# Kernel tuning notes

Hardware: AMD Instinct MI355X
Metric: run time of the kernel (lower is better)

Reference implementation:

```python
import jax, jax.numpy as jnp
import numpy as np

B, T = 64, 32768
N_PROT = 18          # protein channels (len(steady_state))
N_PROLIF = 12        # prolif-hill library terms
N_LIN = 18           # lin-hill library terms (== len(sigmoid_sign))
N_TERMS = 1 + N_PROLIF + N_LIN  # 31


def setup_inputs() -> dict:
    key = jax.random.key(0)
    ks = jax.random.split(key, 8)
    candidates = jax.random.uniform(ks[0], (B, T, 4 + N_PROT), dtype=jnp.float32)
    a = jax.random.normal(ks[1], (N_TERMS,), dtype=jnp.float32)
    steady_state = jax.random.uniform(ks[2], (N_PROT,), dtype=jnp.float32) * 0.5
    # +/-1 signs, mimicking the hard-coded sign vector in the original module
    sigmoid_sign = jnp.where(
        jax.random.bernoulli(ks[3], 0.5, (N_LIN,)), 1.0, -1.0
    ).astype(jnp.float32)
    K1 = jnp.array([0.5], dtype=jnp.float32)
    theta = jnp.array([2.0], dtype=jnp.float32)
    K2 = jnp.array([0.3], dtype=jnp.float32)
    # library indices: cols 0,1 of prolif and col 0 of lin index x (4 channels);
    # col 2 of prolif and col 1 of lin index proteins (18 channels)
    prolif_hill_idx = jnp.stack(
        [
            jax.random.randint(ks[4], (N_PROLIF,), 0, 4),
            jax.random.randint(jax.random.fold_in(ks[4], 1), (N_PROLIF,), 0, 4),
            jax.random.randint(jax.random.fold_in(ks[4], 2), (N_PROLIF,), 0, N_PROT),
        ],
        axis=1,
    ).astype(jnp.int32)
    lin_hill_idx = jnp.stack(
        [
            jax.random.randint(ks[5], (N_LIN,), 0, 4),
            jax.random.randint(jax.random.fold_in(ks[5], 1), (N_LIN,), 0, N_PROT),
        ],
        axis=1,
    ).astype(jnp.int32)
    self_propagate = jax.random.bernoulli(ks[6], 0.5, (N_TERMS,))
    return {
        "candidates": candidates,
        "a": a,
        "steady_state": steady_state,
        "sigmoid_sign": sigmoid_sign,
        "K1": K1,
        "theta": theta,
        "K2": K2,
        "prolif_hill_idx": prolif_hill_idx,
        "lin_hill_idx": lin_hill_idx,
        "self_propagate": self_propagate,
    }


def reference(candidates, a, steady_state, sigmoid_sign, K1, theta, K2,
              prolif_hill_idx, lin_hill_idx, self_propagate):
    con = candidates[:, :, 0:1]                       # [B,T,1]
    x3 = candidates[:, :, 1:4]                        # [B,T,3]
    proteins = candidates[:, :, 4:]                   # [B,T,18]
    d_prot = proteins - steady_state                  # [B,T,18]
    # augment x with its sum -> 4 channels
    x = jnp.concatenate([x3, jnp.sum(x3, axis=2, keepdims=True)], axis=2)

    # prolif-hill terms: Log_term(x_i, x_j) * Hill(K1, protein_k)
    p0 = x[:, :, prolif_hill_idx[:, 0]]
    p1 = x[:, :, prolif_hill_idx[:, 1]]
    p2 = proteins[:, :, prolif_hill_idx[:, 2]]
    prolif_hill = p0 * (1.0 - p1 / theta) * (p2 / (K1 + p2))  # [B,T,12]

    # lin-hill terms: x_i * Hill(K2, |d_prot_j|) * sharp_sigmoid(sign * d_prot_j)
    l0 = x[:, :, lin_hill_idx[:, 0]]
    dp = d_prot[:, :, lin_hill_idx[:, 1]]
    adp = jnp.abs(dp)
    sig = jax.nn.sigmoid(500.0 * (sigmoid_sign * dp - 0.05))
    lin_hill = l0 * (adp / (K2 + adp)) * sig                  # [B,T,18]

    terms = jnp.concatenate([con, prolif_hill, lin_hill], axis=2)  # [B,T,31]

    # masked zero-out: keep term i iff (self_propagate[i] and a[i] >= 0)
    # or (not self_propagate[i] and a[i] <= 0)
    keep = jnp.where(self_propagate, a >= 0.0, a <= 0.0)
    terms = terms * keep.astype(terms.dtype)

    return terms @ a  # [B,T]
```

## Files before the change

### kernel.cpp

```cpp
#include <hip/hip_runtime.h>

#define NPROLIF 12
#define NLIN 18
#define ROW 22
#define BLK 256
#define F4_PER_BLK (BLK*ROW/4)
#define NSLAB 8192

#define AS1 __attribute__((address_space(1)))
#define AS3 __attribute__((address_space(3)))

__device__ __forceinline__ float sel4(unsigned i, float x0, float x1, float x2, float x3) {
    float lo = (i & 1u) ? x1 : x0;
    float hi = (i & 1u) ? x3 : x2;
    return (i & 2u) ? hi : lo;
}

__global__ __launch_bounds__(BLK) void sindy_kernel(
    const float* __restrict__ cand,
    const float* __restrict__ a,
    const float* __restrict__ ss,
    const float* __restrict__ sgn,
    const float* __restrict__ K1p,
    const float* __restrict__ thetap,
    const float* __restrict__ K2p,
    const int* __restrict__ pidx,
    const int* __restrict__ lidx,
    const int* __restrict__ sprop,
    float* __restrict__ out)
{
    __shared__ float sRow[BLK*ROW];
    __shared__ uint2 sPP[NPROLIF];
    __shared__ uint4 sLP[NLIN];
    __shared__ float sScal[4];

    const int tid = threadIdx.x;
    const int wbase = tid & ~63;

    const int slab = ((blockIdx.x & 7) << 10) | (blockIdx.x >> 3);

    const float4* g4 = reinterpret_cast<const float4*>(cand)
                       + (long long)slab * F4_PER_BLK;
    float4* s4 = reinterpret_cast<float4*>(sRow);
    #pragma unroll
    for (int k = 0; k < 5; ++k) {
        __builtin_amdgcn_global_load_lds(
            (const AS1 void*)(g4 + k*BLK + tid),
            (AS3 void*)(s4 + k*BLK + wbase), 16, 0, 0);
    }
    if (tid < F4_PER_BLK - 5*BLK) {
        __builtin_amdgcn_global_load_lds(
            (const AS1 void*)(g4 + 5*BLK + tid),
            (AS3 void*)(s4 + 5*BLK + wbase), 16, 0, 0);
    }

    if (tid < NPROLIF) {
        int i = tid;
        int ia = pidx[i*3+0], ib = pidx[i*3+1], ic = pidx[i*3+2];
        float av = a[1+i];
        bool keep = sprop[1+i] ? (av >= 0.f) : (av <= 0.f);
        unsigned offs = (unsigned)ia | ((unsigned)ib << 2) | ((unsigned)(16 + ic*4) << 8);
        sPP[i] = make_uint2(offs, __float_as_uint(keep ? av : 0.f));
    } else if (tid < NPROLIF + NLIN) {
        int j = tid - NPROLIF;
        int i0 = lidx[j*2+0], i1 = lidx[j*2+1];
        float av = a[1+NPROLIF+j];
        bool keep = sprop[1+NPROLIF+j] ? (av >= 0.f) : (av <= 0.f);
        unsigned offs = (unsigned)i0 | ((unsigned)(16 + i1*4) << 8);
        sLP[j] = make_uint4(offs,
                            __float_as_uint(keep ? av : 0.f),
                            __float_as_uint(500.f * sgn[j]),
                            __float_as_uint(ss[i1]));
    } else if (tid == NPROLIF + NLIN) {
        float av = a[0];
        bool keep = sprop[0] ? (av >= 0.f) : (av <= 0.f);
        sScal[0] = K1p[0];
        sScal[1] = 1.0f / thetap[0];
        sScal[2] = K2p[0];
        sScal[3] = keep ? av : 0.f;
    }

    __syncthreads();

    const char* row = (const char*)&sRow[tid*ROW];
    float con = sRow[tid*ROW+0];
    float x0  = sRow[tid*ROW+1];
    float x1  = sRow[tid*ROW+2];
    float x2  = sRow[tid*ROW+3];
    float xs  = x0 + x1 + x2;

    const float K1 = sScal[0], invTh = sScal[1], K2 = sScal[2];
    float acc = sScal[3] * con;

    #pragma unroll
    for (int i = 0; i < NPROLIF; ++i) {
        uint2 pp = sPP[i];
        float coef = __uint_as_float(pp.y);
        float pA = sel4(pp.x & 3u, x0, x1, x2, xs);
        float pB = sel4((pp.x >> 2) & 3u, x0, x1, x2, xs);
        float pC = *(const float*)(row + ((pp.x >> 8) & 0xffu));
        float h  = pC * __builtin_amdgcn_rcpf(K1 + pC);
        acc += coef * (pA * (1.0f - pB * invTh) * h);
    }

    #pragma unroll
    for (int j = 0; j < NLIN; ++j) {
        uint4 lp = sLP[j];
        float coef = __uint_as_float(lp.y);
        float A    = __uint_as_float(lp.z);
        float ssv  = __uint_as_float(lp.w);
        float l0 = sel4(lp.x & 3u, x0, x1, x2, xs);
        float pr = *(const float*)(row + ((lp.x >> 8) & 0xffu));
        float dp  = pr - ssv;
        float adp = fabsf(dp);
        float h   = adp * __builtin_amdgcn_rcpf(K2 + adp);
        float z   = A * dp - 25.0f;
        float e   = __expf(-z);
        float sig = __builtin_amdgcn_rcpf(1.0f + e);
        acc += coef * (l0 * h * sig);
    }

    out[(long long)slab * BLK + tid] = acc;
}

extern "C" void kernel_launch(void* const* d_in, const int* in_sizes, int n_in,
                              void* d_out, int out_size, void* d_ws, size_t ws_size,
                              hipStream_t stream) {
    const float* cand = (const float*)d_in[0];
    const float* a    = (const float*)d_in[1];
    const float* ss   = (const float*)d_in[2];
    const float* sgn  = (const float*)d_in[3];
    const float* K1   = (const float*)d_in[4];
    const float* th   = (const float*)d_in[5];
    const float* K2   = (const float*)d_in[6];
    const int*   pidx = (const int*)d_in[7];
    const int*   lidx = (const int*)d_in[8];
    const int*   sp   = (const int*)d_in[9];
    float* out = (float*)d_out;

    hipLaunchKernelGGL(sindy_kernel, dim3(NSLAB), dim3(BLK), 0, stream,
                       cand, a, ss, sgn, K1, th, K2, pidx, lidx, sp, out);
}
```

Baseline: 44.55 us.

## Use persistent blocks with register-prefetched next slab overlapping compute

Replaces the one-slab-per-block launch with a fixed grid of persistent blocks that loop over slabs. Each block prefetches the next slab into registers while computing the current one, then copies it to LDS between barriers. This replaces the direct global-to-LDS async loads and drops the blockIdx swizzle. It aims to hide load latency and amortise per-block setup, but adds register pressure and two barriers per iteration.

```diff
diff --git a/kernel.cpp b/kernel.cpp
--- a/kernel.cpp
+++ b/kernel.cpp
@@ -4,11 +4,9 @@
 #define NLIN 18
 #define ROW 22
 #define BLK 256
-#define F4_PER_BLK (BLK*ROW/4)
 #define NSLAB 8192
-
-#define AS1 __attribute__((address_space(1)))
-#define AS3 __attribute__((address_space(3)))
+#define GRID 1536
+#define F4_PER_SLAB (BLK*ROW/4)
 
 __device__ __forceinline__ float sel4(unsigned i, float x0, float x1, float x2, float x3) {
     float lo = (i & 1u) ? x1 : x0;
@@ -35,92 +33,107 @@
     __shared__ float sScal[4];
 
     const int tid = threadIdx.x;
-    const int wbase = tid & ~63;
+    const int bid = blockIdx.x;
 
-    const int slab = ((blockIdx.x & 7) << 10) | (blockIdx.x >> 3);
-
-    const float4* g4 = reinterpret_cast<const float4*>(cand)
-                       + (long long)slab * F4_PER_BLK;
-    float4* s4 = reinterpret_cast<float4*>(sRow);
-    #pragma unroll
-    for (int k = 0; k < 5; ++k) {
-        __builtin_amdgcn_global_load_lds(
-            (const AS1 void*)(g4 + k*BLK + tid),
-            (AS3 void*)(s4 + k*BLK + wbase), 16, 0, 0);
-    }
-    if (tid < F4_PER_BLK - 5*BLK) {
-        __builtin_amdgcn_global_load_lds(
-            (const AS1 void*)(g4 + 5*BLK + tid),
-            (AS3 void*)(s4 + 5*BLK + wbase), 16, 0, 0);
-    }
+    const int niter = (NSLAB - bid + GRID - 1) / GRID;
 
     if (tid < NPROLIF) {
-        int i = tid;
-        int ia = pidx[i*3+0], ib = pidx[i*3+1], ic = pidx[i*3+2];
-        float av = a[1+i];
-        bool keep = sprop[1+i] ? (av >= 0.f) : (av <= 0.f);
+        int t = tid;
+        int ia = pidx[t*3+0], ib = pidx[t*3+1], ic = pidx[t*3+2];
+        unsigned avb  = __float_as_uint(a[1+t]);
+        unsigned keep = ((sprop[1+t] != 0) ? 1u : 0u) ^ (avb >> 31);
         unsigned offs = (unsigned)ia | ((unsigned)ib << 2) | ((unsigned)(16 + ic*4) << 8);
-        sPP[i] = make_uint2(offs, __float_as_uint(keep ? av : 0.f));
+        sPP[t] = make_uint2(offs, keep ? avb : 0u);
     } else if (tid < NPROLIF + NLIN) {
         int j = tid - NPROLIF;
         int i0 = lidx[j*2+0], i1 = lidx[j*2+1];
-        float av = a[1+NPROLIF+j];
-        bool keep = sprop[1+NPROLIF+j] ? (av >= 0.f) : (av <= 0.f);
+        unsigned avb  = __float_as_uint(a[1+NPROLIF+j]);
+        unsigned keep = ((sprop[1+NPROLIF+j] != 0) ? 1u : 0u) ^ (avb >> 31);
         unsigned offs = (unsigned)i0 | ((unsigned)(16 + i1*4) << 8);
-        sLP[j] = make_uint4(offs,
-                            __float_as_uint(keep ? av : 0.f),
-                            __float_as_uint(500.f * sgn[j]),
-                            __float_as_uint(ss[i1]));
+        unsigned A = 0x43fa0000u | (__float_as_uint(sgn[j]) & 0x80000000u);
+        sLP[j] = make_uint4(offs, keep ? avb : 0u, A, __float_as_uint(ss[i1]));
     } else if (tid == NPROLIF + NLIN) {
-        float av = a[0];
-        bool keep = sprop[0] ? (av >= 0.f) : (av <= 0.f);
+        unsigned avb  = __float_as_uint(a[0]);
+        unsigned keep = ((sprop[0] != 0) ? 1u : 0u) ^ (avb >> 31);
         sScal[0] = K1p[0];
-        sScal[1] = 1.0f / thetap[0];
+        sScal[1] = __builtin_amdgcn_rcpf(thetap[0]);
         sScal[2] = K2p[0];
-        sScal[3] = keep ? av : 0.f;
+        sScal[3] = __uint_as_float(keep ? avb : 0u);
     }
 
+    const float4* g4base = reinterpret_cast<const float4*>(cand);
+    float4* s4 = reinterpret_cast<float4*>(sRow);
+    const bool tail = (tid < F4_PER_SLAB - 5*BLK);
+
+    float4 r0, r1, r2, r3, r4, r5;
+    {
+        const float4* g4 = g4base + (long long)bid * F4_PER_SLAB;
+        r0 = g4[tid + 0*BLK]; r1 = g4[tid + 1*BLK]; r2 = g4[tid + 2*BLK];
+        r3 = g4[tid + 3*BLK]; r4 = g4[tid + 4*BLK];
+        if (tail) r5 = g4[tid + 5*BLK];
+    }
+    s4[tid + 0*BLK] = r0; s4[tid + 1*BLK] = r1; s4[tid + 2*BLK] = r2;
+    s4[tid + 3*BLK] = r3; s4[tid + 4*BLK] = r4;
+    if (tail) s4[tid + 5*BLK] = r5;
     __syncthreads();
 
-    const char* row = (const char*)&sRow[tid*ROW];
-    float con = sRow[tid*ROW+0];
-    float x0  = sRow[tid*ROW+1];
-    float x1  = sRow[tid*ROW+2];
-    float x2  = sRow[tid*ROW+3];
-    float xs  = x0 + x1 + x2;
+    const float K1 = sScal[0], invTh = sScal[1], K2 = sScal[2], coef0 = sScal[3];
 
-    const float K1 = sScal[0], invTh = sScal[1], K2 = sScal[2];
-    float acc = sScal[3] * con;
+    for (int i = 0; i < niter; ++i) {
+        if (i + 1 < niter) {
+            const float4* g4 = g4base + (long long)(bid + (i+1)*GRID) * F4_PER_SLAB;
+            r0 = g4[tid + 0*BLK]; r1 = g4[tid + 1*BLK]; r2 = g4[tid + 2*BLK];
+            r3 = g4[tid + 3*BLK]; r4 = g4[tid + 4*BLK];
+            if (tail) r5 = g4[tid + 5*BLK];
+        }
+        __builtin_amdgcn_sched_barrier(0);
 
-    #pragma unroll
-    for (int i = 0; i < NPROLIF; ++i) {
-        uint2 pp = sPP[i];
-        float coef = __uint_as_float(pp.y);
-        float pA = sel4(pp.x & 3u, x0, x1, x2, xs);
-        float pB = sel4((pp.x >> 2) & 3u, x0, x1, x2, xs);
-        float pC = *(const float*)(row + ((pp.x >> 8) & 0xffu));
-        float h  = pC * __builtin_amdgcn_rcpf(K1 + pC);
-        acc += coef * (pA * (1.0f - pB * invTh) * h);
+        const char* row = (const char*)&sRow[tid*ROW];
+        float con = sRow[tid*ROW+0];
+        float x0  = sRow[tid*ROW+1];
+        float x1  = sRow[tid*ROW+2];
+        float x2  = sRow[tid*ROW+3];
+        float xs  = x0 + x1 + x2;
+
+        float acc = coef0 * con;
+
+        #pragma unroll
+        for (int t = 0; t < NPROLIF; ++t) {
+            uint2 pp = sPP[t];
+            float coef = __uint_as_float(pp.y);
+            float pA = sel4(pp.x & 3u, x0, x1, x2, xs);
+            float pB = sel4((pp.x >> 2) & 3u, x0, x1, x2, xs);
+            float pC = *(const float*)(row + ((pp.x >> 8) & 0xffu));
+            float h  = pC * __builtin_amdgcn_rcpf(K1 + pC);
+            acc += coef * (pA * (1.0f - pB * invTh) * h);
+        }
+
+        #pragma unroll
+        for (int t = 0; t < NLIN; ++t) {
+            uint4 lp = sLP[t];
+            float coef = __uint_as_float(lp.y);
+            float A    = __uint_as_float(lp.z);
+            float ssv  = __uint_as_float(lp.w);
+            float l0 = sel4(lp.x & 3u, x0, x1, x2, xs);
+            float pr = *(const float*)(row + ((lp.x >> 8) & 0xffu));
+            float dp  = pr - ssv;
+            float adp = fabsf(dp);
+            float h   = adp * __builtin_amdgcn_rcpf(K2 + adp);
+            float e   = __expf(-(A * dp - 25.0f));
+            float sig = __builtin_amdgcn_rcpf(1.0f + e);
+            acc += coef * (l0 * h * sig);
+        }
+
+        out[(long long)(bid + i*GRID) * BLK + tid] = acc;
+
+        if (i + 1 < niter) {
+            __syncthreads();
+            s4[tid + 0*BLK] = r0; s4[tid + 1*BLK] = r1; s4[tid + 2*BLK] = r2;
+            s4[tid + 3*BLK] = r3; s4[tid + 4*BLK] = r4;
+            if (tail) s4[tid + 5*BLK] = r5;
+            __syncthreads();
+        }
     }
-
-    #pragma unroll
-    for (int j = 0; j < NLIN; ++j) {
-        uint4 lp = sLP[j];
-        float coef = __uint_as_float(lp.y);
-        float A    = __uint_as_float(lp.z);
-        float ssv  = __uint_as_float(lp.w);
-        float l0 = sel4(lp.x & 3u, x0, x1, x2, xs);
-        float pr = *(const float*)(row + ((lp.x >> 8) & 0xffu));
-        float dp  = pr - ssv;
-        float adp = fabsf(dp);
-        float h   = adp * __builtin_amdgcn_rcpf(K2 + adp);
-        float z   = A * dp - 25.0f;
-        float e   = __expf(-z);
-        float sig = __builtin_amdgcn_rcpf(1.0f + e);
-        acc += coef * (l0 * h * sig);
-    }
-
-    out[(long long)slab * BLK + tid] = acc;
 }
 
 extern "C" void kernel_launch(void* const* d_in, const int* in_sizes, int n_in,
@@ -138,6 +151,6 @@
     const int*   sp   = (const int*)d_in[9];
     float* out = (float*)d_out;
 
-    hipLaunchKernelGGL(sindy_kernel, dim3(NSLAB), dim3(BLK), 0, stream,
+    hipLaunchKernelGGL(sindy_kernel, dim3(GRID), dim3(BLK), 0, stream,
                        cand, a, ss, sgn, K1, th, K2, pidx, lidx, sp, out);
 }
```

Measured after the change: 46.18 us. 1.04x slower.

## Precompute term tables in a tiny prologue kernel and read them uniformly from workspace

Applied to the files above, without the earlier changes.

Moves the per-block construction of the term parameter tables into a separate single-block kernel that writes packed words into workspace. The main kernel then reads them through uniform (scalar) loads instead of building shared tables per block. It also drops the XCD-interleaved slab remapping in favour of direct blockIdx indexing. This removes redundant per-block global reads and shared-memory traffic. In exchange it adds a second kernel launch and a dependency between the two launches.

```diff
diff --git a/kernel.cpp b/kernel.cpp
--- a/kernel.cpp
+++ b/kernel.cpp
@@ -10,6 +10,45 @@
 #define AS1 __attribute__((address_space(1)))
 #define AS3 __attribute__((address_space(3)))
 
+
+__global__ void build_tables(const float* __restrict__ a,
+                             const float* __restrict__ ss,
+                             const float* __restrict__ sgn,
+                             const float* __restrict__ K1p,
+                             const float* __restrict__ thetap,
+                             const float* __restrict__ K2p,
+                             const int* __restrict__ pidx,
+                             const int* __restrict__ lidx,
+                             const int* __restrict__ sprop,
+                             unsigned* __restrict__ tw)
+{
+    const int t = threadIdx.x;
+    if (t == 0) {
+        tw[0] = __float_as_uint(K1p[0]);
+        tw[1] = __float_as_uint(__builtin_amdgcn_rcpf(thetap[0]));
+        tw[2] = __float_as_uint(K2p[0]);
+        unsigned avb  = __float_as_uint(a[0]);
+        unsigned keep = ((sprop[0] != 0) ? 1u : 0u) ^ (avb >> 31);
+        tw[3] = keep ? avb : 0u;
+    } else if (t <= NPROLIF) {
+        int i = t - 1;
+        int ia = pidx[i*3+0], ib = pidx[i*3+1], ic = pidx[i*3+2];
+        unsigned avb  = __float_as_uint(a[1+i]);
+        unsigned keep = ((sprop[1+i] != 0) ? 1u : 0u) ^ (avb >> 31);
+        tw[4+2*i] = (unsigned)ia | ((unsigned)ib << 2) | ((unsigned)(16 + ic*4) << 8);
+        tw[5+2*i] = keep ? avb : 0u;
+    } else if (t <= NPROLIF + NLIN) {
+        int j = t - 1 - NPROLIF;
+        int i0 = lidx[j*2+0], i1 = lidx[j*2+1];
+        unsigned avb  = __float_as_uint(a[1+NPROLIF+j]);
+        unsigned keep = ((sprop[1+NPROLIF+j] != 0) ? 1u : 0u) ^ (avb >> 31);
+        tw[28+4*j] = (unsigned)i0 | ((unsigned)(16 + i1*4) << 8);
+        tw[29+4*j] = keep ? avb : 0u;
+        tw[30+4*j] = 0x43fa0000u | (__float_as_uint(sgn[j]) & 0x80000000u);
+        tw[31+4*j] = __float_as_uint(ss[i1]);
+    }
+}
+
 __device__ __forceinline__ float sel4(unsigned i, float x0, float x1, float x2, float x3) {
     float lo = (i & 1u) ? x1 : x0;
     float hi = (i & 1u) ? x3 : x2;
@@ -18,29 +57,16 @@
 
 __global__ __launch_bounds__(BLK) void sindy_kernel(
     const float* __restrict__ cand,
-    const float* __restrict__ a,
-    const float* __restrict__ ss,
-    const float* __restrict__ sgn,
-    const float* __restrict__ K1p,
-    const float* __restrict__ thetap,
-    const float* __restrict__ K2p,
-    const int* __restrict__ pidx,
-    const int* __restrict__ lidx,
-    const int* __restrict__ sprop,
+    const unsigned* __restrict__ tw,
     float* __restrict__ out)
 {
     __shared__ float sRow[BLK*ROW];
-    __shared__ uint2 sPP[NPROLIF];
-    __shared__ uint4 sLP[NLIN];
-    __shared__ float sScal[4];
 
     const int tid = threadIdx.x;
     const int wbase = tid & ~63;
 
-    const int slab = ((blockIdx.x & 7) << 10) | (blockIdx.x >> 3);
-
     const float4* g4 = reinterpret_cast<const float4*>(cand)
-                       + (long long)slab * F4_PER_BLK;
+                       + (long long)blockIdx.x * F4_PER_BLK;
     float4* s4 = reinterpret_cast<float4*>(sRow);
     #pragma unroll
     for (int k = 0; k < 5; ++k) {
@@ -54,32 +80,6 @@
             (AS3 void*)(s4 + 5*BLK + wbase), 16, 0, 0);
     }
 
-    if (tid < NPROLIF) {
-        int i = tid;
-        int ia = pidx[i*3+0], ib = pidx[i*3+1], ic = pidx[i*3+2];
-        float av = a[1+i];
-        bool keep = sprop[1+i] ? (av >= 0.f) : (av <= 0.f);
-        unsigned offs = (unsigned)ia | ((unsigned)ib << 2) | ((unsigned)(16 + ic*4) << 8);
-        sPP[i] = make_uint2(offs, __float_as_uint(keep ? av : 0.f));
-    } else if (tid < NPROLIF + NLIN) {
-        int j = tid - NPROLIF;
-        int i0 = lidx[j*2+0], i1 = lidx[j*2+1];
-        float av = a[1+NPROLIF+j];
-        bool keep = sprop[1+NPROLIF+j] ? (av >= 0.f) : (av <= 0.f);
-        unsigned offs = (unsigned)i0 | ((unsigned)(16 + i1*4) << 8);
-        sLP[j] = make_uint4(offs,
-                            __float_as_uint(keep ? av : 0.f),
-                            __float_as_uint(500.f * sgn[j]),
-                            __float_as_uint(ss[i1]));
-    } else if (tid == NPROLIF + NLIN) {
-        float av = a[0];
-        bool keep = sprop[0] ? (av >= 0.f) : (av <= 0.f);
-        sScal[0] = K1p[0];
-        sScal[1] = 1.0f / thetap[0];
-        sScal[2] = K2p[0];
-        sScal[3] = keep ? av : 0.f;
-    }
-
     __syncthreads();
 
     const char* row = (const char*)&sRow[tid*ROW];
@@ -89,38 +89,39 @@
     float x2  = sRow[tid*ROW+3];
     float xs  = x0 + x1 + x2;
 
-    const float K1 = sScal[0], invTh = sScal[1], K2 = sScal[2];
-    float acc = sScal[3] * con;
+    const float K1    = __uint_as_float(tw[0]);
+    const float invTh = __uint_as_float(tw[1]);
+    const float K2    = __uint_as_float(tw[2]);
+    float acc = __uint_as_float(tw[3]) * con;
 
     #pragma unroll
-    for (int i = 0; i < NPROLIF; ++i) {
-        uint2 pp = sPP[i];
-        float coef = __uint_as_float(pp.y);
-        float pA = sel4(pp.x & 3u, x0, x1, x2, xs);
-        float pB = sel4((pp.x >> 2) & 3u, x0, x1, x2, xs);
-        float pC = *(const float*)(row + ((pp.x >> 8) & 0xffu));
+    for (int t = 0; t < NPROLIF; ++t) {
+        unsigned offs = tw[4+2*t];
+        float coef = __uint_as_float(tw[5+2*t]);
+        float pA = sel4(offs & 3u, x0, x1, x2, xs);
+        float pB = sel4((offs >> 2) & 3u, x0, x1, x2, xs);
+        float pC = *(const float*)(row + ((offs >> 8) & 0xffu));
         float h  = pC * __builtin_amdgcn_rcpf(K1 + pC);
         acc += coef * (pA * (1.0f - pB * invTh) * h);
     }
 
     #pragma unroll
-    for (int j = 0; j < NLIN; ++j) {
-        uint4 lp = sLP[j];
-        float coef = __uint_as_float(lp.y);
-        float A    = __uint_as_float(lp.z);
-        float ssv  = __uint_as_float(lp.w);
-        float l0 = sel4(lp.x & 3u, x0, x1, x2, xs);
-        float pr = *(const float*)(row + ((lp.x >> 8) & 0xffu));
+    for (int t = 0; t < NLIN; ++t) {
+        unsigned offs = tw[28+4*t];
+        float coef = __uint_as_float(tw[29+4*t]);
+        float A    = __uint_as_float(tw[30+4*t]);
+        float ssv  = __uint_as_float(tw[31+4*t]);
+        float l0 = sel4(offs & 3u, x0, x1, x2, xs);
+        float pr = *(const float*)(row + ((offs >> 8) & 0xffu));
         float dp  = pr - ssv;
         float adp = fabsf(dp);
         float h   = adp * __builtin_amdgcn_rcpf(K2 + adp);
-        float z   = A * dp - 25.0f;
-        float e   = __expf(-z);
+        float e   = __expf(-(A * dp - 25.0f));
         float sig = __builtin_amdgcn_rcpf(1.0f + e);
         acc += coef * (l0 * h * sig);
     }
 
-    out[(long long)slab * BLK + tid] = acc;
+    out[(long long)blockIdx.x * BLK + tid] = acc;
 }
 
 extern "C" void kernel_launch(void* const* d_in, const int* in_sizes, int n_in,
@@ -136,8 +137,11 @@
     const int*   pidx = (const int*)d_in[7];
     const int*   lidx = (const int*)d_in[8];
     const int*   sp   = (const int*)d_in[9];
+    unsigned* tw = (unsigned*)d_ws;
     float* out = (float*)d_out;
 
+    hipLaunchKernelGGL(build_tables, dim3(1), dim3(64), 0, stream,
+                       a, ss, sgn, K1, th, K2, pidx, lidx, sp, tw);
     hipLaunchKernelGGL(sindy_kernel, dim3(NSLAB), dim3(BLK), 0, stream,
-                       cand, a, ss, sgn, K1, th, K2, pidx, lidx, sp, out);
+                       cand, tw, out);
 }
```

Result: no change. 44.86 us (+0.7%).
